# Kernel tuning notes

Measured on AMD Instinct MI355X. Metric: run time of the kernel, lower is better.

The kernel has to match this reference:

```python
import jax, jax.numpy as jnp
import numpy as np

D_MODEL = 1024
NUM_HEADS = 16
HEAD_DIM = D_MODEL // NUM_HEADS


def setup_inputs() -> dict:
    key = jax.random.key(0)
    ks = jax.random.split(key, 9)
    B, S = 2, 2048
    s = 1.0 / np.sqrt(D_MODEL)
    inp = {
        "x": jax.random.normal(ks[0], (B, S, D_MODEL), dtype=jnp.float32),
        "Wq": jax.random.normal(ks[1], (D_MODEL, D_MODEL), dtype=jnp.float32) * s,
        "bq": jnp.zeros((D_MODEL,), dtype=jnp.float32),
        "Wk": jax.random.normal(ks[2], (D_MODEL, D_MODEL), dtype=jnp.float32) * s,
        "bk": jnp.zeros((D_MODEL,), dtype=jnp.float32),
        "Wv": jax.random.normal(ks[3], (D_MODEL, D_MODEL), dtype=jnp.float32) * s,
        "bv": jnp.zeros((D_MODEL,), dtype=jnp.float32),
        "Wo": jax.random.normal(ks[4], (D_MODEL, D_MODEL), dtype=jnp.float32) * s,
        "bo": jnp.zeros((D_MODEL,), dtype=jnp.float32),
    }
    return inp


def _rope(x, seq_len):
    # x: [B, H, S, Dh]; rotate-half RoPE with base 10000
    dh = x.shape[-1]
    inv_freq = 1.0 / (10000.0 ** (jnp.arange(0, dh, 2, dtype=jnp.float32) / dh))
    t = jnp.arange(seq_len, dtype=jnp.float32)
    freqs = jnp.einsum("i,j->ij", t, inv_freq)          # [S, Dh/2]
    emb = jnp.concatenate([freqs, freqs], axis=-1)        # [S, Dh]
    cos = jnp.cos(emb)[None, None, :, :]
    sin = jnp.sin(emb)[None, None, :, :]
    x1, x2 = jnp.split(x, 2, axis=-1)
    rot = jnp.concatenate([-x2, x1], axis=-1)
    return x * cos + rot * sin


def reference(x, Wq, bq, Wk, bk, Wv, bv, Wo, bo):
    B, S, _ = x.shape
    H, Dh = NUM_HEADS, HEAD_DIM

    def proj(W, b):
        y = x @ W.T + b                                   # [B, S, D]
        return y.reshape(B, S, H, Dh).transpose(0, 2, 1, 3)  # [B, H, S, Dh]

    q = _rope(proj(Wq, bq), S)
    k = _rope(proj(Wk, bk), S)
    v = proj(Wv, bv)

    scores = jnp.einsum("bhqd,bhkd->bhqk", q, k) / jnp.sqrt(jnp.float32(Dh))
    causal = jnp.triu(jnp.ones((S, S), dtype=bool), k=1)  # True above diag -> masked
    scores = jnp.where(causal[None, None], -jnp.inf, scores)
    attn = jax.nn.softmax(scores, axis=-1)
    out = jnp.einsum("bhqk,bhkd->bhqd", attn, v)          # [B, H, S, Dh]
    out = out.transpose(0, 2, 1, 3).reshape(B, S, H * Dh)
    return out @ Wo.T + bo
```

## Files before the change

kernel.cpp:

```cpp
#include <hip/hip_runtime.h>
#include <math.h>

typedef __bf16 bf16_t;
typedef bf16_t bf16x8 __attribute__((ext_vector_type(8)));
typedef float f32x4 __attribute__((ext_vector_type(4)));

#define S_LEN 2048
#define NHEAD 16
#define DHEAD 64
#define DMODEL 1024
#define BATCH 2

__device__ __forceinline__ float bf2f(unsigned short u) {
    unsigned int x = ((unsigned int)u) << 16;
    return __builtin_bit_cast(float, x);
}
__device__ __forceinline__ unsigned short f2bf(float f) {
    unsigned int x = __builtin_bit_cast(unsigned int, f);
    x += 0x7fffu + ((x >> 16) & 1u);
    return (unsigned short)(x >> 16);
}

__device__ __forceinline__ void glds16(const void* g, void* l) {
    __builtin_amdgcn_global_load_lds(
        (__attribute__((address_space(1))) void*)g,
        (__attribute__((address_space(3))) void*)l,
        16, 0, 0);
}

#define SCALE2 0.1803368801f

__global__ __launch_bounds__(256) void cvt_kernel(
    const float* __restrict__ x,  const float* __restrict__ wq,
    const float* __restrict__ wk, const float* __restrict__ wv,
    const float* __restrict__ wo,
    unsigned short* __restrict__ xb,  unsigned short* __restrict__ wqb,
    unsigned short* __restrict__ wkb, unsigned short* __restrict__ wvb,
    unsigned short* __restrict__ wob)
{
    const int y = blockIdx.y;
    const float* s = (y == 0) ? x : (y == 1) ? wq : (y == 2) ? wk : (y == 3) ? wv : wo;
    unsigned short* d = (y == 0) ? xb : (y == 1) ? wqb : (y == 2) ? wkb : (y == 3) ? wvb : wob;
    const int n4 = (y == 0) ? (1 << 20) : (1 << 18);
    const int i = blockIdx.x * 256 + threadIdx.x;
    if (i < n4) {
        float4 v = ((const float4*)s)[i];
        ushort4 o;
        o.x = f2bf(v.x); o.y = f2bf(v.y); o.z = f2bf(v.z); o.w = f2bf(v.w);
        ((ushort4*)d)[i] = o;
    }
}

__global__ __launch_bounds__(256) void rope_table_kernel(float2* __restrict__ tab)
{
    const int gid = blockIdx.x * 256 + threadIdx.x;
    const int s = gid >> 5, d = gid & 31;
    const float freq = exp2f(-0.4152410119f * (float)d);
    const float ang = (float)s * freq;
    tab[gid] = make_float2(cosf(ang), sinf(ang));
}

__global__ __launch_bounds__(256, 2) void qkv_gemm_kernel(
    const unsigned short* __restrict__ xb,
    const unsigned short* __restrict__ wqb, const unsigned short* __restrict__ wkb,
    const unsigned short* __restrict__ wvb,
    const float* __restrict__ bq, const float* __restrict__ bk, const float* __restrict__ bv,
    const float2* __restrict__ tab,
    unsigned short* __restrict__ Qr, unsigned short* __restrict__ Kr,
    unsigned short* __restrict__ VT)
{
    __shared__ __align__(16) unsigned short As[128 * 32];
    __shared__ __align__(16) unsigned short Bs[128 * 32];

    const int which = blockIdx.x >> 3;
    const int bn = (blockIdx.x & 7) * 128;
    const int bm = blockIdx.y * 128;
    const unsigned short* W = (which == 0) ? wqb : (which == 1) ? wkb : wvb;
    const float* bias       = (which == 0) ? bq  : (which == 1) ? bk  : bv;

    const int tid  = threadIdx.x;
    const int lane = tid & 63;
    const int w    = tid >> 6;
    const int quad = lane >> 4;
    const int l16  = lane & 15;
    const int wm   = (w >> 1) * 64;
    const int wn   = (w & 1) * 64;

    f32x4 acc[4][4];
#pragma unroll
    for (int i = 0; i < 4; ++i)
#pragma unroll
        for (int j = 0; j < 4; ++j)
            acc[i][j] = f32x4{0.f, 0.f, 0.f, 0.f};

    const int r0 = tid >> 2, c0 = (tid & 3) * 8;
    const unsigned short* ga0 = xb + (size_t)(bm + r0) * DMODEL + c0;
    const unsigned short* ga1 = ga0 + (size_t)64 * DMODEL;
    const unsigned short* gb0 = W  + (size_t)(bn + r0) * DMODEL + c0;
    const unsigned short* gb1 = gb0 + (size_t)64 * DMODEL;
    unsigned short* la0 = As + tid * 8;
    unsigned short* la1 = As + (tid + 256) * 8;
    unsigned short* lb0 = Bs + tid * 8;
    unsigned short* lb1 = Bs + (tid + 256) * 8;

    for (int k0 = 0; k0 < DMODEL; k0 += 32) {
        glds16(ga0 + k0, la0);
        glds16(ga1 + k0, la1);
        glds16(gb0 + k0, lb0);
        glds16(gb1 + k0, lb1);
        __syncthreads();

        bf16x8 aF[4], bF[4];
#pragma unroll
        for (int t = 0; t < 4; ++t) {
            aF[t] = *(const bf16x8*)(&As[(wm + t * 16 + l16) * 32 + quad * 8]);
            bF[t] = *(const bf16x8*)(&Bs[(wn + t * 16 + l16) * 32 + quad * 8]);
        }
#pragma unroll
        for (int mt = 0; mt < 4; ++mt)
#pragma unroll
            for (int nt = 0; nt < 4; ++nt)
                acc[mt][nt] = __builtin_amdgcn_mfma_f32_16x16x32_bf16(
                    aF[mt], bF[nt], acc[mt][nt], 0, 0, 0);
        __syncthreads();
    }

    if (which < 2) {
        unsigned short* Y = (which == 0) ? Qr : Kr;
        const float qscale = (which == 0) ? SCALE2 : 1.0f;
#pragma unroll
        for (int mt = 0; mt < 4; ++mt) {
            const int row0 = bm + wm + mt * 16 + quad * 4;
#pragma unroll
            for (int nt = 0; nt < 2; ++nt) {
                const int d   = nt * 16 + l16;
                const int col = bn + wn + nt * 16 + l16;
                const float b1 = bias[col];
                const float b2 = bias[col + 32];
#pragma unroll
                for (int r = 0; r < 4; ++r) {
                    const int row = row0 + r;
                    const int s = row & (S_LEN - 1);
                    const float2 cs = tab[s * 32 + d];
                    const float x1 = acc[mt][nt][r] + b1;
                    const float x2 = acc[mt][nt + 2][r] + b2;
                    Y[(size_t)row * DMODEL + col]      = f2bf((x1 * cs.x - x2 * cs.y) * qscale);
                    Y[(size_t)row * DMODEL + col + 32] = f2bf((x2 * cs.x + x1 * cs.y) * qscale);
                }
            }
        }
    } else {
#pragma unroll
        for (int mt = 0; mt < 4; ++mt) {
            const int row0 = bm + wm + mt * 16 + quad * 4;
            const int bb = row0 >> 11, s0 = row0 & (S_LEN - 1);
            const int h = (bn + wn) >> 6;
#pragma unroll
            for (int nt = 0; nt < 4; ++nt) {
                const int d = nt * 16 + l16;
                const float bv2 = bias[bn + wn + nt * 16 + l16];
                unsigned short pk[4];
#pragma unroll
                for (int r = 0; r < 4; ++r)
                    pk[r] = f2bf(acc[mt][nt][r] + bv2);
                *(uint2*)(&VT[((size_t)(bb * NHEAD + h) * DHEAD + d) * S_LEN + s0]) =
                    *(const uint2*)pk;
            }
        }
    }
}

#define VSTR 136

__global__ __launch_bounds__(256) void attn_kernel(
    const unsigned short* __restrict__ Q, const unsigned short* __restrict__ K,
    const unsigned short* __restrict__ VT, unsigned short* __restrict__ O)
{
    const int qt = gridDim.x - 1 - blockIdx.x;
    const int h  = blockIdx.y;
    const int b  = blockIdx.z;
    const int tid  = threadIdx.x;
    const int w    = tid >> 6;
    const int lane = tid & 63;
    const int quad = lane >> 4;
    const int l16  = lane & 15;

    __shared__ __align__(16) unsigned short Ks[128 * 64];
    __shared__ __align__(16) unsigned short Vt[64 * 128];
    __shared__ __align__(16) unsigned short Pb[4 * 16 * VSTR];

    const int q0 = qt * 128;
    const unsigned short* Qb = Q  + (size_t)b * S_LEN * DMODEL + h * DHEAD;
    const unsigned short* Kb = K  + (size_t)b * S_LEN * DMODEL + h * DHEAD;
    const unsigned short* Vh = VT + ((size_t)(b * NHEAD + h)) * DHEAD * S_LEN;

    bf16x8 qf[2][2];
#pragma unroll
    for (int g = 0; g < 2; ++g) {
        const int qrow = q0 + g * 64 + w * 16 + l16;
        qf[g][0] = *(const bf16x8*)(Qb + (size_t)qrow * DMODEL + quad * 8);
        qf[g][1] = *(const bf16x8*)(Qb + (size_t)qrow * DMODEL + 32 + quad * 8);
    }

    f32x4 o[2][4];
#pragma unroll
    for (int g = 0; g < 2; ++g)
#pragma unroll
        for (int i = 0; i < 4; ++i) o[g][i] = f32x4{0.f, 0.f, 0.f, 0.f};
    float l_i[2][4] = {{0.f, 0.f, 0.f, 0.f}, {0.f, 0.f, 0.f, 0.f}};

    const int nkt = qt + 1;

    for (int kt = 0; kt < nkt; ++kt) {
#pragma unroll
        for (int i = 0; i < 4; ++i) {
            const int ck = tid + i * 256;
            const int krow = ck >> 3, kc = ck & 7;
            glds16(Kb + (size_t)(kt * 128 + krow) * DMODEL + ((kc ^ (krow & 7)) * 8),
                   Ks + ck * 8);
            const int vrow = ck >> 4, vc = ck & 15;
            glds16(Vh + (size_t)vrow * S_LEN + kt * 128 + ((vc ^ (vrow & 15)) * 8),
                   Vt + ck * 8);
        }
        __syncthreads();

        const bool diag = (kt == nkt - 1);
        unsigned short* Pw = &Pb[w * 16 * VSTR];

#pragma unroll
        for (int g = 0; g < 2; ++g) {
            const int kbmax = (diag && g == 0) ? 2 : 4;

            f32x4 sc[8];
#pragma unroll
            for (int nt = 0; nt < 8; ++nt) {
                if (nt >= 2 * kbmax) break;
                const int row = nt * 16 + l16;
                const bf16x8 kf0 = *(const bf16x8*)(&Ks[row * 64 + ((quad ^ (l16 & 7)) * 8)]);
                const bf16x8 kf1 = *(const bf16x8*)(&Ks[row * 64 + (((4 + quad) ^ (l16 & 7)) * 8)]);
                f32x4 a = f32x4{0.f, 0.f, 0.f, 0.f};
                a = __builtin_amdgcn_mfma_f32_16x16x32_bf16(qf[g][0], kf0, a, 0, 0, 0);
                a = __builtin_amdgcn_mfma_f32_16x16x32_bf16(qf[g][1], kf1, a, 0, 0, 0);
                sc[nt] = a;
            }

            if (diag) {
                const int qpos0 = q0 + g * 64 + w * 16 + quad * 4;
#pragma unroll
                for (int nt = 0; nt < 8; ++nt) {
                    if (nt >= 2 * kbmax) break;
                    const int kpos = kt * 128 + nt * 16 + l16;
#pragma unroll
                    for (int r = 0; r < 4; ++r)
                        if (kpos > qpos0 + r) sc[nt][r] = -INFINITY;
                }
            }

#pragma unroll
            for (int nt = 0; nt < 8; ++nt) {
                if (nt >= 2 * kbmax) break;
#pragma unroll
                for (int r = 0; r < 4; ++r) {
                    const float e = exp2f(sc[nt][r]);
                    sc[nt][r] = e;
                    l_i[g][r] += e;
                }
            }

#pragma unroll
            for (int nt = 0; nt < 8; ++nt) {
                if (nt >= 2 * kbmax) break;
#pragma unroll
                for (int r = 0; r < 4; ++r)
                    Pw[(quad * 4 + r) * VSTR + nt * 16 + l16] = f2bf(sc[nt][r]);
            }

            bf16x8 pA[4];
#pragma unroll
            for (int c = 0; c < 4; ++c) {
                if (c >= kbmax) break;
                pA[c] = *(const bf16x8*)(&Pw[l16 * VSTR + c * 32 + quad * 8]);
            }
#pragma unroll
            for (int nt = 0; nt < 4; ++nt) {
                const int row = nt * 16 + l16;
#pragma unroll
                for (int c = 0; c < 4; ++c) {
                    if (c >= kbmax) break;
                    const bf16x8 vF = *(const bf16x8*)(&Vt[row * 128 + (((c * 4 + quad) ^ l16) * 8)]);
                    o[g][nt] = __builtin_amdgcn_mfma_f32_16x16x32_bf16(pA[c], vF, o[g][nt], 0, 0, 0);
                }
            }
        }
        __syncthreads();
    }

#pragma unroll
    for (int g = 0; g < 2; ++g) {
        float linv[4];
#pragma unroll
        for (int r = 0; r < 4; ++r) {
            float rs = l_i[g][r];
#pragma unroll
            for (int msk = 1; msk < 16; msk <<= 1)
                rs += __shfl_xor(rs, msk);
            linv[r] = 1.0f / rs;
        }
        const int spos0 = q0 + g * 64 + w * 16 + quad * 4;
#pragma unroll
        for (int nt = 0; nt < 4; ++nt)
#pragma unroll
            for (int r = 0; r < 4; ++r) {
                const float val = o[g][nt][r] * linv[r];
                O[((size_t)b * S_LEN + spos0 + r) * DMODEL + h * DHEAD + nt * 16 + l16] = f2bf(val);
            }
    }
}

__global__ __launch_bounds__(256, 2) void outproj_kernel(
    const unsigned short* __restrict__ A, const unsigned short* __restrict__ W,
    const float* __restrict__ bias, float* __restrict__ C)
{
    __shared__ __align__(16) unsigned short As[64 * 32];
    __shared__ __align__(16) unsigned short Bs[128 * 32];

    const int tid  = threadIdx.x;
    const int lane = tid & 63;
    const int w    = tid >> 6;
    const int quad = lane >> 4;
    const int l16  = lane & 15;
    const int wm   = (w >> 1) * 32;
    const int wn   = (w & 1) * 64;
    const int bm   = blockIdx.y * 64;
    const int bn   = blockIdx.x * 128;

    f32x4 acc[2][4];
#pragma unroll
    for (int i = 0; i < 2; ++i)
#pragma unroll
        for (int j = 0; j < 4; ++j)
            acc[i][j] = f32x4{0.f, 0.f, 0.f, 0.f};

    const int r0 = tid >> 2, c0 = (tid & 3) * 8;
    const unsigned short* ga  = A + (size_t)(bm + r0) * DMODEL + c0;
    const unsigned short* gb0 = W + (size_t)(bn + r0) * DMODEL + c0;
    const unsigned short* gb1 = gb0 + (size_t)64 * DMODEL;
    unsigned short* la  = As + tid * 8;
    unsigned short* lb0 = Bs + tid * 8;
    unsigned short* lb1 = Bs + (tid + 256) * 8;

    for (int k0 = 0; k0 < DMODEL; k0 += 32) {
        glds16(ga + k0, la);
        glds16(gb0 + k0, lb0);
        glds16(gb1 + k0, lb1);
        __syncthreads();

        bf16x8 aF[2], bF[4];
#pragma unroll
        for (int t = 0; t < 2; ++t)
            aF[t] = *(const bf16x8*)(&As[(wm + t * 16 + l16) * 32 + quad * 8]);
#pragma unroll
        for (int t = 0; t < 4; ++t)
            bF[t] = *(const bf16x8*)(&Bs[(wn + t * 16 + l16) * 32 + quad * 8]);
#pragma unroll
        for (int mt = 0; mt < 2; ++mt)
#pragma unroll
            for (int nt = 0; nt < 4; ++nt)
                acc[mt][nt] = __builtin_amdgcn_mfma_f32_16x16x32_bf16(
                    aF[mt], bF[nt], acc[mt][nt], 0, 0, 0);
        __syncthreads();
    }

#pragma unroll
    for (int mt = 0; mt < 2; ++mt) {
        const int row0 = bm + wm + mt * 16 + quad * 4;
#pragma unroll
        for (int nt = 0; nt < 4; ++nt) {
            const int col = bn + wn + nt * 16 + l16;
            const float bv = bias[col];
#pragma unroll
            for (int r = 0; r < 4; ++r)
                C[(size_t)(row0 + r) * DMODEL + col] = acc[mt][nt][r] + bv;
        }
    }
}

extern "C" void kernel_launch(void* const* d_in, const int* in_sizes, int n_in,
                              void* d_out, int out_size, void* d_ws, size_t ws_size,
                              hipStream_t stream) {
    const float* x  = (const float*)d_in[0];
    const float* Wq = (const float*)d_in[1];
    const float* bq = (const float*)d_in[2];
    const float* Wk = (const float*)d_in[3];
    const float* bk = (const float*)d_in[4];
    const float* Wv = (const float*)d_in[5];
    const float* bv = (const float*)d_in[6];
    const float* Wo = (const float*)d_in[7];
    const float* bo = (const float*)d_in[8];
    float* out = (float*)d_out;

    char* ws = (char*)d_ws;
    const size_t MB = 1 << 20;
    unsigned short* xb  = (unsigned short*)(ws);
    unsigned short* wqb = (unsigned short*)(ws + 8  * MB);
    unsigned short* wkb = (unsigned short*)(ws + 10 * MB);
    unsigned short* wvb = (unsigned short*)(ws + 12 * MB);
    unsigned short* wob = (unsigned short*)(ws + 14 * MB);
    float2*         tab = (float2*)       (ws + 16 * MB);
    unsigned short* Qr  = (unsigned short*)(ws + 17 * MB);
    unsigned short* Kr  = (unsigned short*)(ws + 25 * MB);
    unsigned short* VT  = (unsigned short*)(ws + 33 * MB);
    unsigned short* AO  = (unsigned short*)(ws + 41 * MB);

    const int M = BATCH * S_LEN;

    cvt_kernel<<<dim3(4096, 5), 256, 0, stream>>>(
        x, Wq, Wk, Wv, Wo, xb, wqb, wkb, wvb, wob);

    rope_table_kernel<<<256, 256, 0, stream>>>(tab);

    qkv_gemm_kernel<<<dim3(24, M / 128), 256, 0, stream>>>(
        xb, wqb, wkb, wvb, bq, bk, bv, tab, Qr, Kr, VT);

    attn_kernel<<<dim3(S_LEN / 128, NHEAD, BATCH), 256, 0, stream>>>(Qr, Kr, VT, AO);

    outproj_kernel<<<dim3(DMODEL / 128, M / 64), 256, 0, stream>>>(AO, wob, bo, out);
}
```

Measured before the change: 223.4 us.

## Use 8 waves per attention block and interleave query tiles for balance

The attention kernel goes from 4 waves that each handle two 16-row query groups to 8 waves that each handle one group, doubling the threads per block. This halves per-thread register state and spreads each K/V tile over more waves. The launch becomes a 1D grid whose block-to-query-tile mapping interleaves heavy and light causal tiles and reverses the order for the second batch, to balance work across CUs. The trade-off is a larger shared P buffer and more waves competing at each barrier, which may limit occupancy.

```diff
diff --git a/kernel.cpp b/kernel.cpp
--- a/kernel.cpp
+++ b/kernel.cpp
@@ -172,13 +172,18 @@
 
 #define VSTR 136
 
-__global__ __launch_bounds__(256) void attn_kernel(
+__global__ __launch_bounds__(512, 4) void attn_kernel(
     const unsigned short* __restrict__ Q, const unsigned short* __restrict__ K,
     const unsigned short* __restrict__ VT, unsigned short* __restrict__ O)
 {
-    const int qt = gridDim.x - 1 - blockIdx.x;
-    const int h  = blockIdx.y;
-    const int b  = blockIdx.z;
+    const int j  = blockIdx.x;
+    const int u  = j & 255;
+    const int b  = j >> 8;
+    const int m  = u & 15;
+    int qt = (m & 1) ? (m >> 1) : (15 - (m >> 1));
+    if (b) qt = 15 - qt;
+    const int h  = u >> 4;
+
     const int tid  = threadIdx.x;
     const int w    = tid >> 6;
     const int lane = tid & 63;
@@ -187,34 +192,29 @@
 
     __shared__ __align__(16) unsigned short Ks[128 * 64];
     __shared__ __align__(16) unsigned short Vt[64 * 128];
-    __shared__ __align__(16) unsigned short Pb[4 * 16 * VSTR];
+    __shared__ __align__(16) unsigned short Pb[8 * 16 * VSTR];
 
     const int q0 = qt * 128;
     const unsigned short* Qb = Q  + (size_t)b * S_LEN * DMODEL + h * DHEAD;
     const unsigned short* Kb = K  + (size_t)b * S_LEN * DMODEL + h * DHEAD;
     const unsigned short* Vh = VT + ((size_t)(b * NHEAD + h)) * DHEAD * S_LEN;
 
-    bf16x8 qf[2][2];
-#pragma unroll
-    for (int g = 0; g < 2; ++g) {
-        const int qrow = q0 + g * 64 + w * 16 + l16;
-        qf[g][0] = *(const bf16x8*)(Qb + (size_t)qrow * DMODEL + quad * 8);
-        qf[g][1] = *(const bf16x8*)(Qb + (size_t)qrow * DMODEL + 32 + quad * 8);
-    }
-
-    f32x4 o[2][4];
-#pragma unroll
-    for (int g = 0; g < 2; ++g)
-#pragma unroll
-        for (int i = 0; i < 4; ++i) o[g][i] = f32x4{0.f, 0.f, 0.f, 0.f};
-    float l_i[2][4] = {{0.f, 0.f, 0.f, 0.f}, {0.f, 0.f, 0.f, 0.f}};
+    const int qrow = q0 + w * 16 + l16;
+    const bf16x8 qf0 = *(const bf16x8*)(Qb + (size_t)qrow * DMODEL + quad * 8);
+    const bf16x8 qf1 = *(const bf16x8*)(Qb + (size_t)qrow * DMODEL + 32 + quad * 8);
+
+    f32x4 o[4];
+#pragma unroll
+    for (int i = 0; i < 4; ++i) o[i] = f32x4{0.f, 0.f, 0.f, 0.f};
+    float l_i[4] = {0.f, 0.f, 0.f, 0.f};
 
     const int nkt = qt + 1;
+    unsigned short* Pw = &Pb[w * 16 * VSTR];
 
     for (int kt = 0; kt < nkt; ++kt) {
 #pragma unroll
-        for (int i = 0; i < 4; ++i) {
-            const int ck = tid + i * 256;
+        for (int i = 0; i < 2; ++i) {
+            const int ck = tid + i * 512;
             const int krow = ck >> 3, kc = ck & 7;
             glds16(Kb + (size_t)(kt * 128 + krow) * DMODEL + ((kc ^ (krow & 7)) * 8),
                    Ks + ck * 8);
@@ -225,96 +225,89 @@
         __syncthreads();
 
         const bool diag = (kt == nkt - 1);
-        unsigned short* Pw = &Pb[w * 16 * VSTR];
-
-#pragma unroll
-        for (int g = 0; g < 2; ++g) {
-            const int kbmax = (diag && g == 0) ? 2 : 4;
-
-            f32x4 sc[8];
+        const int ntmax = diag ? ((w & ~1) + 2) : 8;
+        const int cmax  = ntmax >> 1;
+
+        f32x4 sc[8];
+#pragma unroll
+        for (int nt = 0; nt < 8; ++nt) {
+            if (nt >= ntmax) break;
+            const int row = nt * 16 + l16;
+            const bf16x8 kf0 = *(const bf16x8*)(&Ks[row * 64 + ((quad ^ (l16 & 7)) * 8)]);
+            const bf16x8 kf1 = *(const bf16x8*)(&Ks[row * 64 + (((4 + quad) ^ (l16 & 7)) * 8)]);
+            f32x4 a = f32x4{0.f, 0.f, 0.f, 0.f};
+            a = __builtin_amdgcn_mfma_f32_16x16x32_bf16(qf0, kf0, a, 0, 0, 0);
+            a = __builtin_amdgcn_mfma_f32_16x16x32_bf16(qf1, kf1, a, 0, 0, 0);
+            sc[nt] = a;
+        }
+
+        if (diag) {
+            const int qpos0 = q0 + w * 16 + quad * 4;
 #pragma unroll
             for (int nt = 0; nt < 8; ++nt) {
-                if (nt >= 2 * kbmax) break;
-                const int row = nt * 16 + l16;
-                const bf16x8 kf0 = *(const bf16x8*)(&Ks[row * 64 + ((quad ^ (l16 & 7)) * 8)]);
-                const bf16x8 kf1 = *(const bf16x8*)(&Ks[row * 64 + (((4 + quad) ^ (l16 & 7)) * 8)]);
-                f32x4 a = f32x4{0.f, 0.f, 0.f, 0.f};
-                a = __builtin_amdgcn_mfma_f32_16x16x32_bf16(qf[g][0], kf0, a, 0, 0, 0);
-                a = __builtin_amdgcn_mfma_f32_16x16x32_bf16(qf[g][1], kf1, a, 0, 0, 0);
-                sc[nt] = a;
+                if (nt >= ntmax) break;
+                const int kpos = kt * 128 + nt * 16 + l16;
+#pragma unroll
+                for (int r = 0; r < 4; ++r)
+                    if (kpos > qpos0 + r) sc[nt][r] = -INFINITY;
             }
-
-            if (diag) {
-                const int qpos0 = q0 + g * 64 + w * 16 + quad * 4;
-#pragma unroll
-                for (int nt = 0; nt < 8; ++nt) {
-                    if (nt >= 2 * kbmax) break;
-                    const int kpos = kt * 128 + nt * 16 + l16;
-#pragma unroll
-                    for (int r = 0; r < 4; ++r)
-                        if (kpos > qpos0 + r) sc[nt][r] = -INFINITY;
-                }
+        }
+
+#pragma unroll
+        for (int nt = 0; nt < 8; ++nt) {
+            if (nt >= ntmax) break;
+#pragma unroll
+            for (int r = 0; r < 4; ++r) {
+                const float e = exp2f(sc[nt][r]);
+                sc[nt][r] = e;
+                l_i[r] += e;
             }
-
-#pragma unroll
-            for (int nt = 0; nt < 8; ++nt) {
-                if (nt >= 2 * kbmax) break;
-#pragma unroll
-                for (int r = 0; r < 4; ++r) {
-                    const float e = exp2f(sc[nt][r]);
-                    sc[nt][r] = e;
-                    l_i[g][r] += e;
-                }
+        }
+
+#pragma unroll
+        for (int nt = 0; nt < 8; ++nt) {
+            if (nt >= ntmax) break;
+#pragma unroll
+            for (int r = 0; r < 4; ++r)
+                Pw[(quad * 4 + r) * VSTR + nt * 16 + l16] = f2bf(sc[nt][r]);
+        }
+
+        bf16x8 pA[4];
+#pragma unroll
+        for (int c = 0; c < 4; ++c) {
+            if (c >= cmax) break;
+            pA[c] = *(const bf16x8*)(&Pw[l16 * VSTR + c * 32 + quad * 8]);
+        }
+#pragma unroll
+        for (int nt = 0; nt < 4; ++nt) {
+            const int row = nt * 16 + l16;
+#pragma unroll
+            for (int c = 0; c < 4; ++c) {
+                if (c >= cmax) break;
+                const bf16x8 vF = *(const bf16x8*)(&Vt[row * 128 + (((c * 4 + quad) ^ l16) * 8)]);
+                o[nt] = __builtin_amdgcn_mfma_f32_16x16x32_bf16(pA[c], vF, o[nt], 0, 0, 0);
             }
-
-#pragma unroll
-            for (int nt = 0; nt < 8; ++nt) {
-                if (nt >= 2 * kbmax) break;
-#pragma unroll
-                for (int r = 0; r < 4; ++r)
-                    Pw[(quad * 4 + r) * VSTR + nt * 16 + l16] = f2bf(sc[nt][r]);
-            }
-
-            bf16x8 pA[4];
-#pragma unroll
-            for (int c = 0; c < 4; ++c) {
-                if (c >= kbmax) break;
-                pA[c] = *(const bf16x8*)(&Pw[l16 * VSTR + c * 32 + quad * 8]);
-            }
-#pragma unroll
-            for (int nt = 0; nt < 4; ++nt) {
-                const int row = nt * 16 + l16;
-#pragma unroll
-                for (int c = 0; c < 4; ++c) {
-                    if (c >= kbmax) break;
-                    const bf16x8 vF = *(const bf16x8*)(&Vt[row * 128 + (((c * 4 + quad) ^ l16) * 8)]);
-                    o[g][nt] = __builtin_amdgcn_mfma_f32_16x16x32_bf16(pA[c], vF, o[g][nt], 0, 0, 0);
-                }
-            }
-        }
-        __syncthreads();
-    }
-
-#pragma unroll
-    for (int g = 0; g < 2; ++g) {
-        float linv[4];
+        }
+        __syncthreads();
+    }
+
+    float linv[4];
+#pragma unroll
+    for (int r = 0; r < 4; ++r) {
+        float rs = l_i[r];
+#pragma unroll
+        for (int msk = 1; msk < 16; msk <<= 1)
+            rs += __shfl_xor(rs, msk);
+        linv[r] = 1.0f / rs;
+    }
+    const int spos0 = q0 + w * 16 + quad * 4;
+#pragma unroll
+    for (int nt = 0; nt < 4; ++nt)
 #pragma unroll
         for (int r = 0; r < 4; ++r) {
-            float rs = l_i[g][r];
-#pragma unroll
-            for (int msk = 1; msk < 16; msk <<= 1)
-                rs += __shfl_xor(rs, msk);
-            linv[r] = 1.0f / rs;
-        }
-        const int spos0 = q0 + g * 64 + w * 16 + quad * 4;
-#pragma unroll
-        for (int nt = 0; nt < 4; ++nt)
-#pragma unroll
-            for (int r = 0; r < 4; ++r) {
-                const float val = o[g][nt][r] * linv[r];
-                O[((size_t)b * S_LEN + spos0 + r) * DMODEL + h * DHEAD + nt * 16 + l16] = f2bf(val);
-            }
-    }
+            const float val = o[nt][r] * linv[r];
+            O[((size_t)b * S_LEN + spos0 + r) * DMODEL + h * DHEAD + nt * 16 + l16] = f2bf(val);
+        }
 }
 
 __global__ __launch_bounds__(256, 2) void outproj_kernel(
@@ -422,7 +415,7 @@
     qkv_gemm_kernel<<<dim3(24, M / 128), 256, 0, stream>>>(
         xb, wqb, wkb, wvb, bq, bk, bv, tab, Qr, Kr, VT);
 
-    attn_kernel<<<dim3(S_LEN / 128, NHEAD, BATCH), 256, 0, stream>>>(Qr, Kr, VT, AO);
+    attn_kernel<<<dim3(512), 512, 0, stream>>>(Qr, Kr, VT, AO);
 
     outproj_kernel<<<dim3(DMODEL / 128, M / 64), 256, 0, stream>>>(AO, wob, bo, out);
 }
```

After: 198.3 us. -11.2%, faster.
